# Performance work log

Measured on AMD Instinct MI355X. Metric: run time of the kernel, lower is better.

Reference implementation:

```python
import jax, jax.numpy as jnp
import numpy as np
import math
from jax import lax

K = 5
PAD = K // 2
TAU = 0.1
ALPHA = 2.0
BETA = 1.0
MAXH = math.log(K * K - 1)


def _logp(f):
    # f: [B, d, H, W]; normalize along channels, local kxk affinities (center excluded), log_softmax
    B, d, H, W = f.shape
    nrm = jnp.sqrt(jnp.sum(f * f, axis=1, keepdims=True))
    fn = f / jnp.maximum(nrm, 1e-12)
    fp = jnp.pad(fn, ((0, 0), (0, 0), (PAD, PAD), (PAD, PAD)), mode='reflect')
    center = K * K // 2
    affs = []
    for i in range(K):
        for j in range(K):
            if i * K + j == center:
                continue  # mask removes the center neighbor
            affs.append(jnp.einsum('bdhw,bdhw->bhw', fn, fp[:, :, i:i + H, j:j + W]))
    aff = jnp.stack(affs, axis=-1).reshape(B, H * W, K * K - 1)
    return jax.nn.log_softmax(aff / TAU, axis=-1)


def _sobel_mag(x):
    # x: [B, C, H, W] -> [B, H*W] edge magnitude, per-image min-max normalized
    xm = jnp.mean(x, axis=1, keepdims=True)
    kx = jnp.array([[-1., 0., 1.], [-2., 0., 2.], [-1., 0., 1.]], dtype=x.dtype).reshape(1, 1, 3, 3)
    ky = jnp.array([[-1., -2., -1.], [0., 0., 0.], [1., 2., 1.]], dtype=x.dtype).reshape(1, 1, 3, 3)
    dn = ('NCHW', 'OIHW', 'NCHW')
    gx = lax.conv_general_dilated(xm, kx, (1, 1), 'SAME', dimension_numbers=dn)
    gy = lax.conv_general_dilated(xm, ky, (1, 1), 'SAME', dimension_numbers=dn)
    m = jnp.sqrt(gx * gx + gy * gy)[:, 0]
    mn = jnp.min(m, axis=(1, 2), keepdims=True)
    mx = jnp.max(m, axis=(1, 2), keepdims=True)
    m = (m - mn) / (mx - mn + 1e-6)
    return m.reshape(m.shape[0], -1)


def setup_inputs() -> dict:
    key = jax.random.key(0)
    k1, k2, k3, k4 = jax.random.split(key, 4)
    fs3 = jax.random.normal(k1, (8, 256, 64, 64), dtype=jnp.float32)
    ft = jax.random.normal(k2, (8, 512, 32, 32), dtype=jnp.float32)
    Ws = jax.random.normal(k3, (64, 256), dtype=jnp.float32) / np.sqrt(256.0)
    Wt = jax.random.normal(k4, (64, 512), dtype=jnp.float32) / np.sqrt(512.0)
    return {"fs3": fs3, "ft": ft, "Ws": Ws, "Wt": Wt}


def reference(fs3, ft, Ws, Wt):
    B, _, H, W = fs3.shape
    # bilinear, align_corners=False (half-pixel) == jax.image.resize 'bilinear'
    ft_r = jax.image.resize(ft, (ft.shape[0], ft.shape[1], H, W), method='bilinear')
    s = jnp.einsum('oc,bchw->bohw', Ws, fs3)   # 1x1 conv, no bias
    t = jnp.einsum('oc,bchw->bohw', Wt, ft_r)
    t_logp = _logp(t)
    s_logp = _logp(s)
    # gating weights computed under no_grad in the original
    t_logp_ng = lax.stop_gradient(t_logp)
    t_p = jnp.exp(t_logp_ng)
    ent = -jnp.sum(t_p * t_logp_ng, axis=-1)
    w_conf = jnp.clip(1.0 - ent / (MAXH + 1e-12), 0.0, 1.0)
    w_edge = _sobel_mag(lax.stop_gradient(t))
    w = w_conf ** ALPHA * (1.0 + BETA * w_edge)
    # zero out pad-wide border
    m = jnp.pad(jnp.ones((B, H - 2 * PAD, W - 2 * PAD), dtype=fs3.dtype),
                ((0, 0), (PAD, PAD), (PAD, PAD)))
    w = lax.stop_gradient(w * m.reshape(B, -1))
    kl = jnp.sum(t_p * (t_logp - s_logp), axis=-1)
    return jnp.sum(w * kl) / (jnp.sum(w) + 1e-6)
```

## Files before the change

### kernel.cpp

```cpp
#include <hip/hip_runtime.h>
#include <math.h>


#define WS_T32   0u
#define WS_TN    2097152u
#define WS_SN    4194304u
#define WS_TM    6291456u
#define WS_MAG   6324224u
#define WS_WTT   6356992u
#define WS_WST   6389760u
#define WS_MNMX  6406144u
#define WS_ACC   6406160u
#define WS_SLOGP 0u

static __device__ __forceinline__ int reflect_idx(int i, int n) {
  if (i < 0) i = -i;
  if (i >= n) i = 2 * n - 2 - i;
  return i;
}

__global__ __launch_bounds__(256) void k_transw(const float* __restrict__ Wt,
                                                const float* __restrict__ Ws,
                                                float* __restrict__ WtT,
                                                float* __restrict__ WsT,
                                                unsigned int* __restrict__ mnmx,
                                                double* __restrict__ accg) {
  if (blockIdx.x == 0) {
    int t = threadIdx.x;
    if (t < 8) mnmx[t] = 0x7F800000u;
    else if (t < 16) mnmx[t] = 0u;
    else if (t == 16) { accg[0] = 0.0; accg[1] = 0.0; }
  }
  int idx = blockIdx.x * 256 + threadIdx.x;
  if (idx < 32768) {
    int o = idx >> 9, c = idx & 511;
    WtT[c * 64 + o] = Wt[idx];
  } else {
    int j = idx - 32768;
    int o = j >> 8, c = j & 255;
    WsT[c * 64 + o] = Ws[j];
  }
}

__global__ __launch_bounds__(256) void k_gemm_t(const float* __restrict__ ft,
                                                const float* __restrict__ WtT,
                                                float* __restrict__ t32p) {
  const int tid = threadIdx.x;
  const int wvu = __builtin_amdgcn_readfirstlane(tid >> 6);
  const int ln = tid & 63;
  const int p = blockIdx.x * 64 + ln;
  const int b = p >> 10, pix = p & 1023;
  const int cbase = blockIdx.y * 128;
  float ac[16];
#pragma unroll
  for (int i = 0; i < 16; i++) ac[i] = 0.f;
  const float* ftb = ft + ((size_t)b * 512 + cbase) * 1024 + pix;
  const float* wp = WtT + (size_t)cbase * 64 + wvu * 16;
  for (int c = 0; c < 128; c += 4) {
    float v0 = ftb[(size_t)(c + 0) * 1024];
    float v1 = ftb[(size_t)(c + 1) * 1024];
    float v2 = ftb[(size_t)(c + 2) * 1024];
    float v3 = ftb[(size_t)(c + 3) * 1024];
#pragma unroll
    for (int o = 0; o < 16; o++)
      ac[o] += wp[(c + 0) * 64 + o] * v0 + wp[(c + 1) * 64 + o] * v1
             + wp[(c + 2) * 64 + o] * v2 + wp[(c + 3) * 64 + o] * v3;
  }
  float4* outp = (float4*)(t32p + (size_t)blockIdx.y * 524288
                           + ((size_t)b * 1024 + pix) * 64 + wvu * 16);
#pragma unroll
  for (int j = 0; j < 4; j++)
    outp[j] = make_float4(ac[4 * j], ac[4 * j + 1], ac[4 * j + 2], ac[4 * j + 3]);
}

__global__ __launch_bounds__(128) void k_resize_norm(const float* __restrict__ t32p,
                                                     float* __restrict__ tn,
                                                     float* __restrict__ tm) {
  const int p = blockIdx.x * 128 + threadIdx.x;
  const int b = p >> 12, pix = p & 4095;
  const int y = pix >> 6, x = pix & 63;
  float fy = 0.5f * y - 0.25f, fx = 0.5f * x - 0.25f;
  int y0f = (int)floorf(fy), x0f = (int)floorf(fx);
  float wy = fy - (float)y0f, wx = fx - (float)x0f;
  int y1 = min(y0f + 1, 31), x1 = min(x0f + 1, 31);
  int y0 = max(y0f, 0), x0 = max(x0f, 0);
  const int ip[4] = {y0 * 32 + x0, y0 * 32 + x1, y1 * 32 + x0, y1 * 32 + x1};
  const float wg[4] = {(1.f - wy) * (1.f - wx), (1.f - wy) * wx, wy * (1.f - wx), wy * wx};
  float v[64];
#pragma unroll
  for (int i = 0; i < 64; i++) v[i] = 0.f;
#pragma unroll
  for (int q = 0; q < 4; q++) {
    const float* src = t32p + ((size_t)b * 1024 + ip[q]) * 64;
    float wq = wg[q];
#pragma unroll
    for (int part = 0; part < 4; part++) {
      const float4* s4 = (const float4*)(src + (size_t)part * 524288);
#pragma unroll
      for (int cg = 0; cg < 16; cg++) {
        float4 f = s4[cg];
        v[4 * cg + 0] += wq * f.x; v[4 * cg + 1] += wq * f.y;
        v[4 * cg + 2] += wq * f.z; v[4 * cg + 3] += wq * f.w;
      }
    }
  }
  float sum = 0.f, ssq = 0.f;
#pragma unroll
  for (int i = 0; i < 64; i++) { sum += v[i]; ssq += v[i] * v[i]; }
  float rn = 1.f / fmaxf(sqrtf(ssq), 1e-12f);
  float4* tnp = (float4*)(tn + ((size_t)b * 4096 + pix) * 64);
#pragma unroll
  for (int cg = 0; cg < 16; cg++)
    tnp[cg] = make_float4(v[4 * cg] * rn, v[4 * cg + 1] * rn, v[4 * cg + 2] * rn, v[4 * cg + 3] * rn);
  tm[p] = sum * (1.f / 64.f);
}

__global__ __launch_bounds__(128) void k_sobel(const float* __restrict__ tm,
                                               float* __restrict__ mag,
                                               unsigned int* __restrict__ mnmx) {
  const int p = blockIdx.x * 128 + threadIdx.x;
  const int b = p >> 12, pix = p & 4095;
  const int y = pix >> 6, x = pix & 63;
  const float* img = tm + (size_t)b * 4096;
  float v[3][3];
#pragma unroll
  for (int r = -1; r <= 1; r++)
#pragma unroll
    for (int c = -1; c <= 1; c++) {
      int yy = y + r, xx = x + c;
      v[r + 1][c + 1] = (yy >= 0 && yy < 64 && xx >= 0 && xx < 64) ? img[yy * 64 + xx] : 0.f;
    }
  float gx = (v[0][2] - v[0][0]) + 2.f * (v[1][2] - v[1][0]) + (v[2][2] - v[2][0]);
  float gy = (v[2][0] - v[0][0]) + 2.f * (v[2][1] - v[0][1]) + (v[2][2] - v[0][2]);
  float m = sqrtf(gx * gx + gy * gy);
  mag[p] = m;
  unsigned int mu = __float_as_uint(m);
  unsigned int mnu = mu, mxu = mu;
#pragma unroll
  for (int off = 32; off >= 1; off >>= 1) {
    mnu = min(mnu, __shfl_xor(mnu, off));
    mxu = max(mxu, __shfl_xor(mxu, off));
  }
  if ((threadIdx.x & 63) == 0) {
    atomicMin(&mnmx[b], mnu);
    atomicMax(&mnmx[8 + b], mxu);
  }
}

__global__ __launch_bounds__(256) void k_gemm_s(const float* __restrict__ fs3,
                                                const float* __restrict__ WsT,
                                                float* __restrict__ sn) {
  __shared__ float ssq_l[4][64];
  const int tid = threadIdx.x;
  const int wvu = __builtin_amdgcn_readfirstlane(tid >> 6);
  const int ln = tid & 63;
  const int p = blockIdx.x * 64 + ln;
  const int b = p >> 12, pix = p & 4095;
  float ac[16];
#pragma unroll
  for (int i = 0; i < 16; i++) ac[i] = 0.f;
  const float* fb = fs3 + (size_t)b * 256 * 4096 + pix;
  const float* wp = WsT + wvu * 16;
  for (int c = 0; c < 256; c += 4) {
    float v0 = fb[(size_t)(c + 0) * 4096];
    float v1 = fb[(size_t)(c + 1) * 4096];
    float v2 = fb[(size_t)(c + 2) * 4096];
    float v3 = fb[(size_t)(c + 3) * 4096];
#pragma unroll
    for (int o = 0; o < 16; o++)
      ac[o] += wp[(c + 0) * 64 + o] * v0 + wp[(c + 1) * 64 + o] * v1
             + wp[(c + 2) * 64 + o] * v2 + wp[(c + 3) * 64 + o] * v3;
  }
  float ss = 0.f;
#pragma unroll
  for (int i = 0; i < 16; i++) ss += ac[i] * ac[i];
  ssq_l[wvu][ln] = ss;
  __syncthreads();
  float tot = ssq_l[0][ln] + ssq_l[1][ln] + ssq_l[2][ln] + ssq_l[3][ln];
  float rn = 1.f / fmaxf(sqrtf(tot), 1e-12f);
  float4* ob = (float4*)(sn + ((size_t)b * 4096 + pix) * 64 + wvu * 16);
#pragma unroll
  for (int j = 0; j < 4; j++)
    ob[j] = make_float4(ac[4 * j] * rn, ac[4 * j + 1] * rn, ac[4 * j + 2] * rn, ac[4 * j + 3] * rn);
}

template <int TPASS>
__global__ __launch_bounds__(256) void k_aff(const float* __restrict__ fn,
                                             float* __restrict__ slogp,
                                             const float* __restrict__ mag,
                                             const unsigned int* __restrict__ mnmx,
                                             double* __restrict__ accg) {
  __shared__ __align__(16) float fl[144 * 68];
  const int tid = threadIdx.x;
  const int wvu = __builtin_amdgcn_readfirstlane(tid >> 6);
  const int ln = tid & 63;
  const int b = blockIdx.x >> 6, tl = blockIdx.x & 63;
  const int ty0 = (tl >> 3) * 8, tx0 = (tl & 7) * 8;
  const int ty = ln >> 3, tx = ln & 7;
#pragma unroll
  for (int i = 0; i < 9; i++) {
    int flat = i * 256 + tid;
    int pos = flat >> 4, cg = flat & 15;
    int hy = pos / 12, hx = pos - hy * 12;
    int gy2 = reflect_idx(ty0 + hy - 2, 64);
    int gx2 = reflect_idx(tx0 + hx - 2, 64);
    float4 f = *(const float4*)(fn + ((size_t)b * 4096 + gy2 * 64 + gx2) * 64 + cg * 4);
    int sw = (((pos * 17) >> 3) & 3) << 2;
    *(float4*)(&fl[pos * 68 + ((cg * 4) ^ sw)]) = f;
  }
  __syncthreads();
  const int base = ty * 12 + tx;
  const int cbase = wvu * 16;
  float4 cv[4];
  {
    int cp = base + 26;
    int cs = (((cp * 17) >> 3) & 3) << 2;
    const float* crow = &fl[cp * 68];
#pragma unroll
    for (int j = 0; j < 4; j++) cv[j] = *(const float4*)(crow + ((cbase + 4 * j) ^ cs));
  }
  float aff[24];
  {
    int n = 0;
#pragma unroll
    for (int dy = 0; dy < 5; dy++)
#pragma unroll
      for (int dx = 0; dx < 5; dx++) {
        if (dy == 2 && dx == 2) continue;
        int pp = base + dy * 12 + dx;
        int sw2 = (((pp * 17) >> 3) & 3) << 2;
        const float* rowp = &fl[pp * 68];
        float4 n0 = *(const float4*)(rowp + ((cbase + 0) ^ sw2));
        float4 n1 = *(const float4*)(rowp + ((cbase + 4) ^ sw2));
        float4 n2 = *(const float4*)(rowp + ((cbase + 8) ^ sw2));
        float4 n3 = *(const float4*)(rowp + ((cbase + 12) ^ sw2));
        aff[n] = cv[0].x * n0.x + cv[0].y * n0.y + cv[0].z * n0.z + cv[0].w * n0.w
               + cv[1].x * n1.x + cv[1].y * n1.y + cv[1].z * n1.z + cv[1].w * n1.w
               + cv[2].x * n2.x + cv[2].y * n2.y + cv[2].z * n2.z + cv[2].w * n2.w
               + cv[3].x * n3.x + cv[3].y * n3.y + cv[3].z * n3.z + cv[3].w * n3.w;
        n++;
      }
  }
  __syncthreads();
  float* r = fl;
#pragma unroll
  for (int n = 0; n < 24; n++) r[(wvu * 64 + ln) * 25 + n] = aff[n];
  __syncthreads();
  if (wvu != 0) return;
  float a[24];
#pragma unroll
  for (int n = 0; n < 24; n++)
    a[n] = r[ln * 25 + n] + r[(64 + ln) * 25 + n] + r[(128 + ln) * 25 + n] + r[(192 + ln) * 25 + n];
  float mxa = a[0];
#pragma unroll
  for (int n = 1; n < 24; n++) mxa = fmaxf(mxa, a[n]);
  float e[24]; float sum = 0.f;
#pragma unroll
  for (int n = 0; n < 24; n++) { e[n] = expf((a[n] - mxa) * 10.f); sum += e[n]; }
  float lse = logf(sum);
  const int gy = ty0 + ty, gx = tx0 + tx;
  const int gpix = b * 4096 + gy * 64 + gx;
  if (TPASS == 0) {
#pragma unroll
    for (int n = 0; n < 24; n++)
      slogp[(size_t)n * 32768 + gpix] = (a[n] - mxa) * 10.f - lse;
  } else {
    float rs = 1.f / sum;
    float ent = 0.f, kl = 0.f;
#pragma unroll
    for (int n = 0; n < 24; n++) {
      float tp = e[n] * rs;
      float tlp = (a[n] - mxa) * 10.f - lse;
      ent -= tp * tlp;
      kl += tp * (tlp - slogp[(size_t)n * 32768 + gpix]);
    }
    float wconf = 1.f - ent * (1.0f / 3.17805383034794580f);
    wconf = fminf(fmaxf(wconf, 0.f), 1.f);
    float mnv = __uint_as_float(mnmx[b]);
    float mxv = __uint_as_float(mnmx[8 + b]);
    float wedge = (mag[gpix] - mnv) / (mxv - mnv + 1e-6f);
    float w = wconf * wconf * (1.f + wedge);
    if (gy < 2 || gy >= 62 || gx < 2 || gx >= 62) w = 0.f;
    double wkl = (double)(w * kl), wsum = (double)w;
#pragma unroll
    for (int off = 32; off >= 1; off >>= 1) {
      wkl  += __shfl_down(wkl, off);
      wsum += __shfl_down(wsum, off);
    }
    if (ln == 0) { atomicAdd(&accg[0], wkl); atomicAdd(&accg[1], wsum); }
  }
}

__global__ void k_final(const double* __restrict__ accg, float* __restrict__ out) {
  out[0] = (float)(accg[0] / (accg[1] + 1e-6));
}

extern "C" void kernel_launch(void* const* d_in, const int* in_sizes, int n_in,
                              void* d_out, int out_size, void* d_ws, size_t ws_size,
                              hipStream_t stream) {
  const float* fs3 = (const float*)d_in[0];
  const float* ft  = (const float*)d_in[1];
  const float* Ws  = (const float*)d_in[2];
  const float* Wt  = (const float*)d_in[3];
  float* out = (float*)d_out;
  float* w = (float*)d_ws;
  float* t32   = w + WS_T32;
  float* tn    = w + WS_TN;
  float* sn    = w + WS_SN;
  float* tm    = w + WS_TM;
  float* mag   = w + WS_MAG;
  float* WtT   = w + WS_WTT;
  float* WsT   = w + WS_WST;
  float* slogp = w + WS_SLOGP;
  unsigned int* mnmx = (unsigned int*)(w + WS_MNMX);
  double* acc = (double*)(w + WS_ACC);

  k_transw<<<192, 256, 0, stream>>>(Wt, Ws, WtT, WsT, mnmx, acc);
  k_gemm_t<<<dim3(128, 4), 256, 0, stream>>>(ft, WtT, t32);
  k_resize_norm<<<256, 128, 0, stream>>>(t32, tn, tm);
  k_sobel<<<256, 128, 0, stream>>>(tm, mag, mnmx);
  k_gemm_s<<<512, 256, 0, stream>>>(fs3, WsT, sn);
  k_aff<0><<<512, 256, 0, stream>>>(sn, slogp, nullptr, nullptr, nullptr);
  k_aff<1><<<512, 256, 0, stream>>>(tn, slogp, mag, mnmx, acc);
  k_final<<<1, 1, 0, stream>>>(acc, out);
}
```

Before: 201.4 us.

## Split GEMM channel reduction across waves, drop weight transpose kernel, halve resize work

Removes the weight-transpose kernel and has the 1x1-conv GEMMs read the original row-major weights directly, with wave-uniform scalar-style weight loads. Each GEMM block now uses 512 threads, and two wave groups each take half the input channels and combine their partials through swizzled shared memory. The student GEMM also computes two pixels per thread with float2 loads, and both GEMMs software-prefetch the next activation rows. The resize/normalize kernel splits each pixel's 64 channels across two threads joined by a shuffle, which cuts register pressure, and it absorbs the accumulator initialization. The cost is extra LDS traffic and syncs, and the weight reads become strided rather than contiguous.

```diff
diff --git a/kernel.cpp b/kernel.cpp
--- a/kernel.cpp
+++ b/kernel.cpp
@@ -3,14 +3,12 @@
 
 
 #define WS_T32   0u
-#define WS_TN    2097152u
-#define WS_SN    4194304u
-#define WS_TM    6291456u
-#define WS_MAG   6324224u
-#define WS_WTT   6356992u
-#define WS_WST   6389760u
-#define WS_MNMX  6406144u
-#define WS_ACC   6406160u
+#define WS_TN    1048576u
+#define WS_SN    3145728u
+#define WS_TM    5242880u
+#define WS_MAG   5275648u
+#define WS_MNMX  5308416u
+#define WS_ACC   5308432u
 #define WS_SLOGP 0u
 
 static __device__ __forceinline__ int reflect_idx(int i, int n) {
@@ -19,64 +17,72 @@
   return i;
 }
 
-__global__ __launch_bounds__(256) void k_transw(const float* __restrict__ Wt,
-                                                const float* __restrict__ Ws,
-                                                float* __restrict__ WtT,
-                                                float* __restrict__ WsT,
-                                                unsigned int* __restrict__ mnmx,
-                                                double* __restrict__ accg) {
+__global__ __launch_bounds__(512, 2) void k_gemm_t(const float* __restrict__ ft,
+                                                   const float* __restrict__ Wt,
+                                                   float* __restrict__ t32p) {
+  __shared__ __align__(16) float red[4 * 64 * 20];
+  const int tid = threadIdx.x;
+  const int w = tid >> 6, ln = tid & 63;
+  const int o = w & 3;
+  const int wq = __builtin_amdgcn_readfirstlane(w >> 2);
+  const int obase = __builtin_amdgcn_readfirstlane(o * 16);
+  const int P0 = blockIdx.x * 64;
+  const int b = P0 >> 10;
+  const int pixl = (P0 & 1023) + ln;
+  const int ky = blockIdx.y;
+  float ac[16];
+#pragma unroll
+  for (int i = 0; i < 16; i++) ac[i] = 0.f;
+  const float* fb = ft + (size_t)b * 524288 + (size_t)(ky * 256 + wq * 128) * 1024 + pixl;
+  const float* wb = Wt + obase * 512 + ky * 256 + wq * 128;
+  float n0 = fb[0], n1 = fb[1024], n2 = fb[2048], n3 = fb[3072];
+  for (int c = 0; c < 128; c += 4) {
+    float v0 = n0, v1 = n1, v2 = n2, v3 = n3;
+    if (c + 4 < 128) {
+      const float* nf = fb + (size_t)(c + 4) * 1024;
+      n0 = nf[0]; n1 = nf[1024]; n2 = nf[2048]; n3 = nf[3072];
+    }
+#pragma unroll
+    for (int oo = 0; oo < 16; oo++) {
+      const float* wr = wb + oo * 512 + c;
+      float w0 = wr[0], w1 = wr[1], w2 = wr[2], w3 = wr[3];
+      ac[oo] += w0 * v0 + w1 * v1 + w2 * v2 + w3 * v3;
+    }
+  }
+  if (w >= 4) {
+#pragma unroll
+    for (int j = 0; j < 4; j++)
+      *(float4*)&red[(o * 64 + ln) * 20 + ((j * 4) ^ ((ln & 3) << 2))] =
+          make_float4(ac[4 * j], ac[4 * j + 1], ac[4 * j + 2], ac[4 * j + 3]);
+  }
+  __syncthreads();
+  if (w < 4) {
+#pragma unroll
+    for (int j = 0; j < 4; j++) {
+      float4 r = *(const float4*)&red[(o * 64 + ln) * 20 + ((j * 4) ^ ((ln & 3) << 2))];
+      ac[4 * j] += r.x; ac[4 * j + 1] += r.y; ac[4 * j + 2] += r.z; ac[4 * j + 3] += r.w;
+    }
+    float* outp = t32p + (size_t)ky * 524288 + ((size_t)b * 1024 + pixl) * 64 + obase;
+#pragma unroll
+    for (int j = 0; j < 4; j++)
+      *(float4*)(outp + 4 * j) =
+          make_float4(ac[4 * j], ac[4 * j + 1], ac[4 * j + 2], ac[4 * j + 3]);
+  }
+}
+
+__global__ __launch_bounds__(256) void k_resize_norm(const float* __restrict__ t32p,
+                                                     float* __restrict__ tn,
+                                                     float* __restrict__ tm,
+                                                     unsigned int* __restrict__ mnmx,
+                                                     double* __restrict__ accg) {
   if (blockIdx.x == 0) {
     int t = threadIdx.x;
     if (t < 8) mnmx[t] = 0x7F800000u;
     else if (t < 16) mnmx[t] = 0u;
     else if (t == 16) { accg[0] = 0.0; accg[1] = 0.0; }
   }
-  int idx = blockIdx.x * 256 + threadIdx.x;
-  if (idx < 32768) {
-    int o = idx >> 9, c = idx & 511;
-    WtT[c * 64 + o] = Wt[idx];
-  } else {
-    int j = idx - 32768;
-    int o = j >> 8, c = j & 255;
-    WsT[c * 64 + o] = Ws[j];
-  }
-}
-
-__global__ __launch_bounds__(256) void k_gemm_t(const float* __restrict__ ft,
-                                                const float* __restrict__ WtT,
-                                                float* __restrict__ t32p) {
-  const int tid = threadIdx.x;
-  const int wvu = __builtin_amdgcn_readfirstlane(tid >> 6);
-  const int ln = tid & 63;
-  const int p = blockIdx.x * 64 + ln;
-  const int b = p >> 10, pix = p & 1023;
-  const int cbase = blockIdx.y * 128;
-  float ac[16];
-#pragma unroll
-  for (int i = 0; i < 16; i++) ac[i] = 0.f;
-  const float* ftb = ft + ((size_t)b * 512 + cbase) * 1024 + pix;
-  const float* wp = WtT + (size_t)cbase * 64 + wvu * 16;
-  for (int c = 0; c < 128; c += 4) {
-    float v0 = ftb[(size_t)(c + 0) * 1024];
-    float v1 = ftb[(size_t)(c + 1) * 1024];
-    float v2 = ftb[(size_t)(c + 2) * 1024];
-    float v3 = ftb[(size_t)(c + 3) * 1024];
-#pragma unroll
-    for (int o = 0; o < 16; o++)
-      ac[o] += wp[(c + 0) * 64 + o] * v0 + wp[(c + 1) * 64 + o] * v1
-             + wp[(c + 2) * 64 + o] * v2 + wp[(c + 3) * 64 + o] * v3;
-  }
-  float4* outp = (float4*)(t32p + (size_t)blockIdx.y * 524288
-                           + ((size_t)b * 1024 + pix) * 64 + wvu * 16);
-#pragma unroll
-  for (int j = 0; j < 4; j++)
-    outp[j] = make_float4(ac[4 * j], ac[4 * j + 1], ac[4 * j + 2], ac[4 * j + 3]);
-}
-
-__global__ __launch_bounds__(128) void k_resize_norm(const float* __restrict__ t32p,
-                                                     float* __restrict__ tn,
-                                                     float* __restrict__ tm) {
-  const int p = blockIdx.x * 128 + threadIdx.x;
+  const int g = blockIdx.x * 256 + threadIdx.x;
+  const int p = g >> 1, h = g & 1;
   const int b = p >> 12, pix = p & 4095;
   const int y = pix >> 6, x = pix & 63;
   float fy = 0.5f * y - 0.25f, fx = 0.5f * x - 0.25f;
@@ -86,18 +92,18 @@
   int y0 = max(y0f, 0), x0 = max(x0f, 0);
   const int ip[4] = {y0 * 32 + x0, y0 * 32 + x1, y1 * 32 + x0, y1 * 32 + x1};
   const float wg[4] = {(1.f - wy) * (1.f - wx), (1.f - wy) * wx, wy * (1.f - wx), wy * wx};
-  float v[64];
-#pragma unroll
-  for (int i = 0; i < 64; i++) v[i] = 0.f;
-#pragma unroll
-  for (int q = 0; q < 4; q++) {
-    const float* src = t32p + ((size_t)b * 1024 + ip[q]) * 64;
-    float wq = wg[q];
-#pragma unroll
-    for (int part = 0; part < 4; part++) {
-      const float4* s4 = (const float4*)(src + (size_t)part * 524288);
-#pragma unroll
-      for (int cg = 0; cg < 16; cg++) {
+  float v[32];
+#pragma unroll
+  for (int i = 0; i < 32; i++) v[i] = 0.f;
+#pragma unroll
+  for (int qd = 0; qd < 4; qd++) {
+    float wq = wg[qd];
+#pragma unroll
+    for (int part = 0; part < 2; part++) {
+      const float4* s4 = (const float4*)(t32p + (size_t)part * 524288
+                                         + ((size_t)b * 1024 + ip[qd]) * 64 + h * 32);
+#pragma unroll
+      for (int cg = 0; cg < 8; cg++) {
         float4 f = s4[cg];
         v[4 * cg + 0] += wq * f.x; v[4 * cg + 1] += wq * f.y;
         v[4 * cg + 2] += wq * f.z; v[4 * cg + 3] += wq * f.w;
@@ -106,13 +112,16 @@
   }
   float sum = 0.f, ssq = 0.f;
 #pragma unroll
-  for (int i = 0; i < 64; i++) { sum += v[i]; ssq += v[i] * v[i]; }
-  float rn = 1.f / fmaxf(sqrtf(ssq), 1e-12f);
-  float4* tnp = (float4*)(tn + ((size_t)b * 4096 + pix) * 64);
-#pragma unroll
-  for (int cg = 0; cg < 16; cg++)
-    tnp[cg] = make_float4(v[4 * cg] * rn, v[4 * cg + 1] * rn, v[4 * cg + 2] * rn, v[4 * cg + 3] * rn);
-  tm[p] = sum * (1.f / 64.f);
+  for (int i = 0; i < 32; i++) { sum += v[i]; ssq += v[i] * v[i]; }
+  float sumf = sum + __shfl_xor(sum, 1);
+  float ssqf = ssq + __shfl_xor(ssq, 1);
+  float rn = 1.f / fmaxf(sqrtf(ssqf), 1e-12f);
+  float4* tnp = (float4*)(tn + ((size_t)b * 4096 + pix) * 64 + h * 32);
+#pragma unroll
+  for (int cg = 0; cg < 8; cg++)
+    tnp[cg] = make_float4(v[4 * cg] * rn, v[4 * cg + 1] * rn,
+                          v[4 * cg + 2] * rn, v[4 * cg + 3] * rn);
+  if (h == 0) tm[p] = sumf * (1.f / 64.f);
 }
 
 __global__ __launch_bounds__(128) void k_sobel(const float* __restrict__ tm,
@@ -147,41 +156,84 @@
   }
 }
 
-__global__ __launch_bounds__(256) void k_gemm_s(const float* __restrict__ fs3,
-                                                const float* __restrict__ WsT,
-                                                float* __restrict__ sn) {
-  __shared__ float ssq_l[4][64];
+__global__ __launch_bounds__(512, 2) void k_gemm_s(const float* __restrict__ fs3,
+                                                   const float* __restrict__ Ws,
+                                                   float* __restrict__ sn) {
+  __shared__ __align__(16) float red[4 * 64 * 36];
+  __shared__ float ssq_l[4][132];
   const int tid = threadIdx.x;
-  const int wvu = __builtin_amdgcn_readfirstlane(tid >> 6);
-  const int ln = tid & 63;
-  const int p = blockIdx.x * 64 + ln;
-  const int b = p >> 12, pix = p & 4095;
-  float ac[16];
-#pragma unroll
-  for (int i = 0; i < 16; i++) ac[i] = 0.f;
-  const float* fb = fs3 + (size_t)b * 256 * 4096 + pix;
-  const float* wp = WsT + wvu * 16;
-  for (int c = 0; c < 256; c += 4) {
-    float v0 = fb[(size_t)(c + 0) * 4096];
-    float v1 = fb[(size_t)(c + 1) * 4096];
-    float v2 = fb[(size_t)(c + 2) * 4096];
-    float v3 = fb[(size_t)(c + 3) * 4096];
-#pragma unroll
-    for (int o = 0; o < 16; o++)
-      ac[o] += wp[(c + 0) * 64 + o] * v0 + wp[(c + 1) * 64 + o] * v1
-             + wp[(c + 2) * 64 + o] * v2 + wp[(c + 3) * 64 + o] * v3;
-  }
-  float ss = 0.f;
-#pragma unroll
-  for (int i = 0; i < 16; i++) ss += ac[i] * ac[i];
-  ssq_l[wvu][ln] = ss;
-  __syncthreads();
-  float tot = ssq_l[0][ln] + ssq_l[1][ln] + ssq_l[2][ln] + ssq_l[3][ln];
-  float rn = 1.f / fmaxf(sqrtf(tot), 1e-12f);
-  float4* ob = (float4*)(sn + ((size_t)b * 4096 + pix) * 64 + wvu * 16);
-#pragma unroll
-  for (int j = 0; j < 4; j++)
-    ob[j] = make_float4(ac[4 * j] * rn, ac[4 * j + 1] * rn, ac[4 * j + 2] * rn, ac[4 * j + 3] * rn);
+  const int w = tid >> 6, ln = tid & 63;
+  const int o = w & 3;
+  const int wq = __builtin_amdgcn_readfirstlane(w >> 2);
+  const int obase = __builtin_amdgcn_readfirstlane(o * 16);
+  const int P0 = blockIdx.x * 128;
+  const int b = P0 >> 12;
+  const int pix0 = (P0 & 4095) + 2 * ln;
+  float ac[2][16];
+#pragma unroll
+  for (int i = 0; i < 16; i++) { ac[0][i] = 0.f; ac[1][i] = 0.f; }
+  const float* fb = fs3 + (size_t)b * 1048576 + (size_t)(wq * 128) * 4096 + pix0;
+  const float* wb = Ws + obase * 256 + wq * 128;
+  float2 n0 = *(const float2*)(fb);
+  float2 n1 = *(const float2*)(fb + 4096);
+  float2 n2 = *(const float2*)(fb + 8192);
+  float2 n3 = *(const float2*)(fb + 12288);
+  for (int c = 0; c < 128; c += 4) {
+    float2 v0 = n0, v1 = n1, v2 = n2, v3 = n3;
+    if (c + 4 < 128) {
+      const float* nf = fb + (size_t)(c + 4) * 4096;
+      n0 = *(const float2*)(nf);
+      n1 = *(const float2*)(nf + 4096);
+      n2 = *(const float2*)(nf + 8192);
+      n3 = *(const float2*)(nf + 12288);
+    }
+#pragma unroll
+    for (int oo = 0; oo < 16; oo++) {
+      const float* wr = wb + oo * 256 + c;
+      float w0 = wr[0], w1 = wr[1], w2 = wr[2], w3 = wr[3];
+      ac[0][oo] += w0 * v0.x + w1 * v1.x + w2 * v2.x + w3 * v3.x;
+      ac[1][oo] += w0 * v0.y + w1 * v1.y + w2 * v2.y + w3 * v3.y;
+    }
+  }
+  if (w >= 4) {
+#pragma unroll
+    for (int p2 = 0; p2 < 2; p2++)
+#pragma unroll
+      for (int j = 0; j < 4; j++)
+        *(float4*)&red[(o * 64 + ln) * 36 + (((p2 * 16 + j * 4)) ^ ((ln & 7) << 2))] =
+            make_float4(ac[p2][4 * j], ac[p2][4 * j + 1], ac[p2][4 * j + 2], ac[p2][4 * j + 3]);
+  }
+  __syncthreads();
+  float ss0 = 0.f, ss1 = 0.f;
+  if (w < 4) {
+#pragma unroll
+    for (int p2 = 0; p2 < 2; p2++)
+#pragma unroll
+      for (int j = 0; j < 4; j++) {
+        float4 r = *(const float4*)&red[(o * 64 + ln) * 36 + (((p2 * 16 + j * 4)) ^ ((ln & 7) << 2))];
+        ac[p2][4 * j] += r.x; ac[p2][4 * j + 1] += r.y;
+        ac[p2][4 * j + 2] += r.z; ac[p2][4 * j + 3] += r.w;
+      }
+#pragma unroll
+    for (int i = 0; i < 16; i++) { ss0 += ac[0][i] * ac[0][i]; ss1 += ac[1][i] * ac[1][i]; }
+    ssq_l[o][2 * ln] = ss0;
+    ssq_l[o][2 * ln + 1] = ss1;
+  }
+  __syncthreads();
+  if (w < 4) {
+    float t0 = ssq_l[0][2 * ln] + ssq_l[1][2 * ln] + ssq_l[2][2 * ln] + ssq_l[3][2 * ln];
+    float t1 = ssq_l[0][2 * ln + 1] + ssq_l[1][2 * ln + 1] + ssq_l[2][2 * ln + 1] + ssq_l[3][2 * ln + 1];
+    float rn0 = 1.f / fmaxf(sqrtf(t0), 1e-12f);
+    float rn1 = 1.f / fmaxf(sqrtf(t1), 1e-12f);
+    float* ob = sn + ((size_t)b * 4096 + pix0) * 64 + obase;
+#pragma unroll
+    for (int j = 0; j < 4; j++) {
+      *(float4*)(ob + 4 * j) = make_float4(ac[0][4 * j] * rn0, ac[0][4 * j + 1] * rn0,
+                                           ac[0][4 * j + 2] * rn0, ac[0][4 * j + 3] * rn0);
+      *(float4*)(ob + 64 + 4 * j) = make_float4(ac[1][4 * j] * rn1, ac[1][4 * j + 1] * rn1,
+                                                ac[1][4 * j + 2] * rn1, ac[1][4 * j + 3] * rn1);
+    }
+  }
 }
 
 template <int TPASS>
@@ -230,14 +282,14 @@
         int pp = base + dy * 12 + dx;
         int sw2 = (((pp * 17) >> 3) & 3) << 2;
         const float* rowp = &fl[pp * 68];
-        float4 n0 = *(const float4*)(rowp + ((cbase + 0) ^ sw2));
-        float4 n1 = *(const float4*)(rowp + ((cbase + 4) ^ sw2));
-        float4 n2 = *(const float4*)(rowp + ((cbase + 8) ^ sw2));
-        float4 n3 = *(const float4*)(rowp + ((cbase + 12) ^ sw2));
-        aff[n] = cv[0].x * n0.x + cv[0].y * n0.y + cv[0].z * n0.z + cv[0].w * n0.w
-               + cv[1].x * n1.x + cv[1].y * n1.y + cv[1].z * n1.z + cv[1].w * n1.w
-               + cv[2].x * n2.x + cv[2].y * n2.y + cv[2].z * n2.z + cv[2].w * n2.w
-               + cv[3].x * n3.x + cv[3].y * n3.y + cv[3].z * n3.z + cv[3].w * n3.w;
+        float4 q0 = *(const float4*)(rowp + ((cbase + 0) ^ sw2));
+        float4 q1 = *(const float4*)(rowp + ((cbase + 4) ^ sw2));
+        float4 q2 = *(const float4*)(rowp + ((cbase + 8) ^ sw2));
+        float4 q3 = *(const float4*)(rowp + ((cbase + 12) ^ sw2));
+        aff[n] = cv[0].x * q0.x + cv[0].y * q0.y + cv[0].z * q0.z + cv[0].w * q0.w
+               + cv[1].x * q1.x + cv[1].y * q1.y + cv[1].z * q1.z + cv[1].w * q1.w
+               + cv[2].x * q2.x + cv[2].y * q2.y + cv[2].z * q2.z + cv[2].w * q2.w
+               + cv[3].x * q3.x + cv[3].y * q3.y + cv[3].z * q3.z + cv[3].w * q3.w;
         n++;
       }
   }
@@ -279,9 +331,9 @@
     float mnv = __uint_as_float(mnmx[b]);
     float mxv = __uint_as_float(mnmx[8 + b]);
     float wedge = (mag[gpix] - mnv) / (mxv - mnv + 1e-6f);
-    float w = wconf * wconf * (1.f + wedge);
-    if (gy < 2 || gy >= 62 || gx < 2 || gx >= 62) w = 0.f;
-    double wkl = (double)(w * kl), wsum = (double)w;
+    float wgt = wconf * wconf * (1.f + wedge);
+    if (gy < 2 || gy >= 62 || gx < 2 || gx >= 62) wgt = 0.f;
+    double wkl = (double)(wgt * kl), wsum = (double)wgt;
 #pragma unroll
     for (int off = 32; off >= 1; off >>= 1) {
       wkl  += __shfl_down(wkl, off);
@@ -309,17 +361,14 @@
   float* sn    = w + WS_SN;
   float* tm    = w + WS_TM;
   float* mag   = w + WS_MAG;
-  float* WtT   = w + WS_WTT;
-  float* WsT   = w + WS_WST;
   float* slogp = w + WS_SLOGP;
   unsigned int* mnmx = (unsigned int*)(w + WS_MNMX);
   double* acc = (double*)(w + WS_ACC);
 
-  k_transw<<<192, 256, 0, stream>>>(Wt, Ws, WtT, WsT, mnmx, acc);
-  k_gemm_t<<<dim3(128, 4), 256, 0, stream>>>(ft, WtT, t32);
-  k_resize_norm<<<256, 128, 0, stream>>>(t32, tn, tm);
+  k_gemm_t<<<dim3(128, 2), 512, 0, stream>>>(ft, Wt, t32);
+  k_resize_norm<<<256, 256, 0, stream>>>(t32, tn, tm, mnmx, acc);
   k_sobel<<<256, 128, 0, stream>>>(tm, mag, mnmx);
-  k_gemm_s<<<512, 256, 0, stream>>>(fs3, WsT, sn);
+  k_gemm_s<<<256, 512, 0, stream>>>(fs3, Ws, sn);
   k_aff<0><<<512, 256, 0, stream>>>(sn, slogp, nullptr, nullptr, nullptr);
   k_aff<1><<<512, 256, 0, stream>>>(tn, slogp, mag, mnmx, acc);
   k_final<<<1, 1, 0, stream>>>(acc, out);
```

Measured after the change: 204.0 us. No clear change (+1.3%).
